# Optimization experiments

Measured on AMD Instinct MI355X. Metric: run time of the kernel, lower is better.

The kernel has to match this reference:

```python
import jax, jax.numpy as jnp
import numpy as np

HID = 64; N_LAYERS = 4; N_HEADS = 4; HEAD_DIM = 16; INTER = 32; MAXP = 1024; EPS = 1e-12


def setup_inputs() -> dict:
    key = jax.random.key(0)
    ks = iter(jax.random.split(key, 32))
    rn = lambda shape, s=0.02: jax.random.normal(next(ks), shape, jnp.float32) * s
    B, L = 32, 1024
    return {
        "features": jax.random.normal(next(ks), (B, L, HID), jnp.float32),
        "Wq": rn((N_LAYERS, HID, HID)), "bq": jnp.zeros((N_LAYERS, HID), jnp.float32),
        "Wk": rn((N_LAYERS, HID, HID)), "bk": jnp.zeros((N_LAYERS, HID), jnp.float32),
        "Wv": rn((N_LAYERS, HID, HID)), "bv": jnp.zeros((N_LAYERS, HID), jnp.float32),
        "Wo": rn((N_LAYERS, HID, HID)), "bo": jnp.zeros((N_LAYERS, HID), jnp.float32),
        "ln1_g": jnp.ones((N_LAYERS, HID), jnp.float32), "ln1_b": jnp.zeros((N_LAYERS, HID), jnp.float32),
        "Wi": rn((N_LAYERS, HID, INTER)), "bi": jnp.zeros((N_LAYERS, INTER), jnp.float32),
        "Wd": rn((N_LAYERS, INTER, HID)), "bd": jnp.zeros((N_LAYERS, HID), jnp.float32),
        "ln2_g": jnp.ones((N_LAYERS, HID), jnp.float32), "ln2_b": jnp.zeros((N_LAYERS, HID), jnp.float32),
        "rel_emb": rn((N_LAYERS, 2 * MAXP - 1, HEAD_DIM)),
        "fc_w": rn((HID, 6)), "fc_b": jnp.zeros((6,), jnp.float32),
    }


def _ln(x, g, b):
    m = jnp.mean(x, axis=-1, keepdims=True)
    v = jnp.mean((x - m) ** 2, axis=-1, keepdims=True)
    return (x - m) / jnp.sqrt(v + EPS) * g + b


def reference(features, Wq, bq, Wk, bk, Wv, bv, Wo, bo, ln1_g, ln1_b,
              Wi, bi, Wd, bd, ln2_g, ln2_b, rel_emb, fc_w, fc_b):
    B, L, _ = features.shape
    pos = jnp.arange(L)
    dist_idx = pos[:, None] - pos[None, :] + (MAXP - 1)  # [L, L] in [0, 2*MAXP-2]
    scale = np.float32(1.0 / np.sqrt(HEAD_DIM))

    def heads(t):  # [B,L,HID] -> [B,H,L,D]
        return t.reshape(B, L, N_HEADS, HEAD_DIM).transpose(0, 2, 1, 3)

    x = features
    for i in range(N_LAYERS):
        q = heads(x @ Wq[i] + bq[i])
        k = heads(x @ Wk[i] + bk[i])
        v = heads(x @ Wv[i] + bv[i])
        scores = jnp.einsum("bhld,bhrd->bhlr", q, k)
        pe = rel_emb[i][dist_idx]  # [L, L, D] relative_key positional embedding
        scores = scores + jnp.einsum("bhld,lrd->bhlr", q, pe)
        probs = jax.nn.softmax(scores * scale, axis=-1)
        ctx = jnp.einsum("bhlr,bhrd->bhld", probs, v).transpose(0, 2, 1, 3).reshape(B, L, HID)
        x = _ln(ctx @ Wo[i] + bo[i] + x, ln1_g[i], ln1_b[i])
        inter = jax.nn.gelu(x @ Wi[i] + bi[i], approximate=False)
        x = _ln(inter @ Wd[i] + bd[i] + x, ln2_g[i], ln2_b[i])
    return (x @ fc_w + fc_b)[:, 1:, :]
```

## Files before the change

kernel.cpp:

```cpp
#include <hip/hip_runtime.h>
#include <math.h>

static constexpr int Bc = 32;
static constexpr int Lc = 1024;

typedef _Float16 f16x4 __attribute__((ext_vector_type(4)));
typedef __fp16   h16x2 __attribute__((ext_vector_type(2)));
typedef float    f32x4 __attribute__((ext_vector_type(4)));

#define MFMA16(a, b, c) __builtin_amdgcn_mfma_f32_16x16x16f16((a), (b), (c), 0, 0, 0)

#if __has_builtin(__builtin_amdgcn_exp2f)
#define EXP2(x) __builtin_amdgcn_exp2f(x)
#else
#define EXP2(x) exp2f(x)
#endif

__global__ __launch_bounds__(256) void prep_kernel(
    const float* __restrict__ features, const float* __restrict__ rel,
    const float* __restrict__ Wq, const float* __restrict__ Wk,
    const float* __restrict__ Wv, const float* __restrict__ Wo,
    const float* __restrict__ Wi, const float* __restrict__ Wd,
    _Float16* __restrict__ xh, _Float16* __restrict__ relh,
    _Float16* __restrict__ wt)
{
    int i = blockIdx.x * 256 + threadIdx.x;
    {
        float4 v = ((const float4*)features)[i];
        h16x2 a = __builtin_amdgcn_cvt_pkrtz(v.x, v.y);
        h16x2 b = __builtin_amdgcn_cvt_pkrtz(v.z, v.w);
        f16x4 o; o[0] = a[0]; o[1] = a[1]; o[2] = b[0]; o[3] = b[1];
        ((f16x4*)xh)[i] = o;
    }
    if (i < 32752) {
        float4 v = ((const float4*)rel)[i];
        h16x2 a = __builtin_amdgcn_cvt_pkrtz(v.x, v.y);
        h16x2 b = __builtin_amdgcn_cvt_pkrtz(v.z, v.w);
        f16x4 o; o[0] = a[0]; o[1] = a[1]; o[2] = b[0]; o[3] = b[1];
        ((f16x4*)relh)[i] = o;
    }
    if (i < 65536) {
        int which = i >> 14, r = i & 16383;
        int m = r >> 12, k = (r >> 6) & 63, c = r & 63;
        const float* src = which == 0 ? Wq : which == 1 ? Wk : which == 2 ? Wv : Wo;
        wt[which * 16384 + m * 4096 + c * 64 + k] = (_Float16)src[r];
    } else if (i < 73728) {
        int r = i - 65536;
        int m = r >> 11, k = (r >> 5) & 63, c = r & 31;
        wt[65536 + m * 2048 + c * 64 + k] = (_Float16)Wi[r];
    } else if (i < 81920) {
        int r = i - 73728;
        int m = r >> 11, k = (r >> 6) & 31, c = r & 63;
        wt[73728 + m * 2048 + c * 32 + k] = (_Float16)Wd[r];
    }
}

__global__ __launch_bounds__(256) void qkv_kernel(
    const _Float16* __restrict__ xh,
    const _Float16* __restrict__ qT, const _Float16* __restrict__ kT,
    const _Float16* __restrict__ vT,
    const float* __restrict__ bq, const float* __restrict__ bk,
    const float* __restrict__ bv,
    _Float16* __restrict__ qo, _Float16* __restrict__ ko, _Float16* __restrict__ vt)
{
    const int t = threadIdx.x, wv = t >> 6, lane = t & 63, lo = lane & 15, hi = lane >> 4;
    const int row0 = blockIdx.x * 64 + wv * 16;
    const int b = row0 >> 10, l0 = row0 & 1023;

    f16x4 a[4];
    #pragma unroll
    for (int kk = 0; kk < 4; kk++)
        a[kk] = *(const f16x4*)(xh + (row0 + lo) * 64 + kk * 16 + 4 * hi);

    #pragma unroll
    for (int m = 0; m < 3; m++) {
        const _Float16* WT = m == 0 ? qT : m == 1 ? kT : vT;
        const float* bias  = m == 0 ? bq : m == 1 ? bk : bv;
        #pragma unroll
        for (int h = 0; h < 4; h++) {
            float bb = bias[h * 16 + lo];
            f32x4 acc = { bb, bb, bb, bb };
            #pragma unroll
            for (int kk = 0; kk < 4; kk++) {
                f16x4 bf = *(const f16x4*)(WT + (h * 16 + lo) * 64 + kk * 16 + 4 * hi);
                acc = MFMA16(a[kk], bf, acc);
            }
            int bh = b * 4 + h;
            if (m < 2) {
                _Float16* dst = (m == 0 ? qo : ko) + (bh * Lc + l0 + 4 * hi) * 16 + lo;
                dst[0]  = (_Float16)acc[0];
                dst[16] = (_Float16)acc[1];
                dst[32] = (_Float16)acc[2];
                dst[48] = (_Float16)acc[3];
            } else {
                h16x2 p0 = __builtin_amdgcn_cvt_pkrtz(acc[0], acc[1]);
                h16x2 p1 = __builtin_amdgcn_cvt_pkrtz(acc[2], acc[3]);
                f16x4 o; o[0] = p0[0]; o[1] = p0[1]; o[2] = p1[0]; o[3] = p1[1];
                *(f16x4*)(vt + (bh * 16 + lo) * Lc + l0 + 4 * hi) = o;
            }
        }
    }
}

__global__ __launch_bounds__(64) void attn_kernel(
    const _Float16* __restrict__ qg, const _Float16* __restrict__ kg,
    const _Float16* __restrict__ vtg, const _Float16* __restrict__ relh,
    _Float16* __restrict__ ctxh)
{
    __shared__ float Tl[4][16 * 52];
    const int lane = threadIdx.x & 63;
    const int bh = blockIdx.x & 127;
    const int l0 = (blockIdx.x >> 7) * 64;
    const int lo = lane & 15, hi = lane >> 4;

    const _Float16 qscale = (_Float16)0.36067376022224085f;
    f16x4 qf[4];
    #pragma unroll
    for (int i = 0; i < 4; i++) {
        qf[i] = *(const f16x4*)(qg + (bh * Lc + l0 + 16 * i + lo) * 16 + 4 * hi);
        #pragma unroll
        for (int j = 0; j < 4; j++) qf[i][j] *= qscale;
    }

    const int o = 12 + lo - 4 * hi;

    float* wrE[4]; float* wrO[4]; const float* rdE[4]; const float* rdO[4];
    #pragma unroll
    for (int i = 0; i < 4; i++) {
        float* ring = Tl[i];
        const int phiE = 16 * (i & 1);
        const int phiO = 16 - phiE;
        wrE[i] = ring + lo * 52 + phiE + 4 * hi;
        wrO[i] = ring + lo * 52 + phiO + 4 * hi;
        rdE[i] = ring + lo * 52 + phiE + o;
        rdO[i] = ring + lo * 52 + phiO + o;
    }

    const _Float16* rbase = relh + 4 * hi;
    auto ldrel = [&](int row) {
        row = row > 2046 ? 2046 : row;
        return *(const f16x4*)(rbase + row * 16);
    };
    auto t_store = [&](f16x4 rf, f16x4 q, float* wr, bool mir) {
        f32x4 z = { 0.f, 0.f, 0.f, 0.f };
        f32x4 tt = MFMA16(rf, q, z);
        *(f32x4*)(wr) = tt;
        if (mir) *(f32x4*)(wr + 32) = tt;
    };

    f16x4 P[6];
    #pragma unroll
    for (int k = 0; k < 6; k++) P[k] = ldrel(l0 + 16 * k + lo);
    #pragma unroll
    for (int i = 0; i < 4; i++) {
        t_store(P[i],     qf[i], wrE[i], (i & 1) == 0);
        t_store(P[i + 1], qf[i], wrO[i], (i & 1) == 1);
    }
    f16x4 rc0 = P[2], rc1 = P[3], rc2 = P[4], rc3 = P[5];
    int rrow = l0 + 96 + lo;

    f32x4 si[4];
    #pragma unroll
    for (int i = 0; i < 4; i++) {
        const float* rd = rdE[i];
        si[i][0] = rd[3]; si[i][1] = rd[2]; si[i][2] = rd[1]; si[i][3] = rd[0];
    }

    const _Float16* kp = kg  + (bh * Lc + 1008 + lo) * 16 + 4 * hi;
    const _Float16* vp = vtg + (bh * 16 + lo) * Lc + 1008 + 4 * hi;
    f16x4 kf0 = *(const f16x4*)kp;
    f16x4 vf0 = *(const f16x4*)vp;
    kp -= 256; vp -= 16;
    f16x4 kf1 = *(const f16x4*)kp;
    f16x4 vf1 = *(const f16x4*)vp;

    f32x4 ot[4], d[4];
    #pragma unroll
    for (int i = 0; i < 4; i++) {
        ot[i] = f32x4{ 0.f, 0.f, 0.f, 0.f };
        d[i]  = f32x4{ 0.f, 0.f, 0.f, 0.f };
    }

    #pragma unroll 2
    for (int t = 0; t < 64; ++t) {
        kp -= 256; vp -= 16;
        f16x4 kf2 = *(const f16x4*)kp;
        f16x4 vf2 = *(const f16x4*)vp;
        f16x4 r4 = ldrel(rrow); rrow += 16;

        f32x4 s[4];
        #pragma unroll
        for (int i = 0; i < 4; i++)
            s[i] = MFMA16(kf0, qf[i], si[i]);

        float e[4][4];
        #pragma unroll
        for (int i = 0; i < 4; i++)
            #pragma unroll
            for (int j = 0; j < 4; j++) {
                e[i][j] = EXP2(s[i][j]);
                d[i][j] += e[i][j];
            }

        t_store(rc0, qf[0], (t & 1) ? wrO[0] : wrE[0], (t & 1) == 0);
        t_store(rc1, qf[1], (t & 1) ? wrO[1] : wrE[1], (t & 1) == 1);
        t_store(rc2, qf[2], (t & 1) ? wrO[2] : wrE[2], (t & 1) == 0);
        t_store(rc3, qf[3], (t & 1) ? wrO[3] : wrE[3], (t & 1) == 1);

        #pragma unroll
        for (int i = 0; i < 4; i++) {
            const float* rd = (t & 1) ? rdE[i] : rdO[i];
            si[i][0] = rd[3]; si[i][1] = rd[2]; si[i][2] = rd[1]; si[i][3] = rd[0];
        }

        #pragma unroll
        for (int i = 0; i < 4; i++) {
            h16x2 pa = __builtin_amdgcn_cvt_pkrtz(e[i][0], e[i][1]);
            h16x2 pb = __builtin_amdgcn_cvt_pkrtz(e[i][2], e[i][3]);
            f16x4 pf; pf[0] = pa[0]; pf[1] = pa[1]; pf[2] = pb[0]; pf[3] = pb[1];
            ot[i] = MFMA16(vf0, pf, ot[i]);
        }

        kf0 = kf1; kf1 = kf2;
        vf0 = vf1; vf1 = vf2;
        rc0 = rc1; rc1 = rc2; rc2 = rc3; rc3 = r4;
    }

    const int b = bh >> 2, h = bh & 3;
    #pragma unroll
    for (int i = 0; i < 4; i++) {
        float den = (d[i][0] + d[i][1]) + (d[i][2] + d[i][3]);
        den += __shfl_xor(den, 16);
        den += __shfl_xor(den, 32);
        const float inv = 1.f / den;
        h16x2 o0 = __builtin_amdgcn_cvt_pkrtz(ot[i][0] * inv, ot[i][1] * inv);
        h16x2 o1 = __builtin_amdgcn_cvt_pkrtz(ot[i][2] * inv, ot[i][3] * inv);
        f16x4 o4; o4[0] = o0[0]; o4[1] = o0[1]; o4[2] = o1[0]; o4[3] = o1[1];
        *(f16x4*)(ctxh + (b * Lc + l0 + 16 * i + lo) * 64 + h * 16 + 4 * hi) = o4;
    }
}

__global__ __launch_bounds__(256) void tail_kernel(
    const _Float16* __restrict__ ctxh, const float* __restrict__ resid,
    const _Float16* __restrict__ woT, const float* __restrict__ bo,
    const float* __restrict__ g1, const float* __restrict__ b1,
    const _Float16* __restrict__ wiT, const float* __restrict__ bi,
    const _Float16* __restrict__ wdT, const float* __restrict__ bd,
    const float* __restrict__ g2, const float* __restrict__ b2,
    float* __restrict__ xout,
    int doq,
    const _Float16* __restrict__ qT, const _Float16* __restrict__ kT,
    const _Float16* __restrict__ vT,
    const float* __restrict__ bq, const float* __restrict__ bk,
    const float* __restrict__ bv,
    _Float16* __restrict__ qo, _Float16* __restrict__ ko, _Float16* __restrict__ vt)
{
    __shared__ _Float16 x1s[4][16 * 68];
    __shared__ _Float16 ins[4][16 * 36];
    const int t = threadIdx.x, wv = t >> 6, lane = t & 63, lo = lane & 15, hi = lane >> 4;
    const int row0 = blockIdx.x * 64 + wv * 16;

    f16x4 a[4];
    #pragma unroll
    for (int kk = 0; kk < 4; kk++)
        a[kk] = *(const f16x4*)(ctxh + (row0 + lo) * 64 + kk * 16 + 4 * hi);

    float c1[4][4];
    #pragma unroll
    for (int w = 0; w < 4; w++) {
        float bb = bo[w * 16 + lo];
        f32x4 acc;
        #pragma unroll
        for (int j = 0; j < 4; j++)
            acc[j] = bb + resid[(row0 + 4 * hi + j) * 64 + w * 16 + lo];
        #pragma unroll
        for (int kk = 0; kk < 4; kk++) {
            f16x4 bf = *(const f16x4*)(woT + (w * 16 + lo) * 64 + kk * 16 + 4 * hi);
            acc = MFMA16(a[kk], bf, acc);
        }
        #pragma unroll
        for (int j = 0; j < 4; j++) c1[w][j] = acc[j];
    }

    float x1[4][4];
    {
        float gg[4], bb2[4];
        #pragma unroll
        for (int w = 0; w < 4; w++) { gg[w] = g1[w * 16 + lo]; bb2[w] = b1[w * 16 + lo]; }
        #pragma unroll
        for (int j = 0; j < 4; j++) {
            float s = c1[0][j] + c1[1][j] + c1[2][j] + c1[3][j];
            float q = c1[0][j]*c1[0][j] + c1[1][j]*c1[1][j] + c1[2][j]*c1[2][j] + c1[3][j]*c1[3][j];
            #pragma unroll
            for (int off = 1; off < 16; off <<= 1) { s += __shfl_xor(s, off); q += __shfl_xor(q, off); }
            float m  = s * (1.f / 64.f);
            float vr = q * (1.f / 64.f) - m * m;
            float rs = rsqrtf(vr + 1e-12f);
            #pragma unroll
            for (int w = 0; w < 4; w++) x1[w][j] = (c1[w][j] - m) * rs * gg[w] + bb2[w];
        }
    }

    _Float16* xsp = x1s[wv];
    #pragma unroll
    for (int w = 0; w < 4; w++)
        #pragma unroll
        for (int j = 0; j < 4; j++)
            xsp[(4 * hi + j) * 68 + w * 16 + lo] = (_Float16)x1[w][j];
    f16x4 a2[4];
    #pragma unroll
    for (int kk = 0; kk < 4; kk++)
        a2[kk] = *(const f16x4*)(xsp + lo * 68 + kk * 16 + 4 * hi);

    float it[2][4];
    #pragma unroll
    for (int w = 0; w < 2; w++) {
        float bb = bi[w * 16 + lo];
        f32x4 acc = { bb, bb, bb, bb };
        #pragma unroll
        for (int kk = 0; kk < 4; kk++) {
            f16x4 bf = *(const f16x4*)(wiT + (w * 16 + lo) * 64 + kk * 16 + 4 * hi);
            acc = MFMA16(a2[kk], bf, acc);
        }
        #pragma unroll
        for (int j = 0; j < 4; j++) {
            float v = acc[j];
            it[w][j] = 0.5f * v * (1.f + erff(v * 0.70710678118654752f));
        }
    }

    _Float16* isp = ins[wv];
    #pragma unroll
    for (int w = 0; w < 2; w++)
        #pragma unroll
        for (int j = 0; j < 4; j++)
            isp[(4 * hi + j) * 36 + w * 16 + lo] = (_Float16)it[w][j];
    f16x4 a3[2];
    #pragma unroll
    for (int kk = 0; kk < 2; kk++)
        a3[kk] = *(const f16x4*)(isp + lo * 36 + kk * 16 + 4 * hi);

    float c2[4][4];
    #pragma unroll
    for (int w = 0; w < 4; w++) {
        float bb = bd[w * 16 + lo];
        f32x4 acc;
        #pragma unroll
        for (int j = 0; j < 4; j++) acc[j] = bb + x1[w][j];
        #pragma unroll
        for (int kk = 0; kk < 2; kk++) {
            f16x4 bf = *(const f16x4*)(wdT + (w * 16 + lo) * 32 + kk * 16 + 4 * hi);
            acc = MFMA16(a3[kk], bf, acc);
        }
        #pragma unroll
        for (int j = 0; j < 4; j++) c2[w][j] = acc[j];
    }

    float x2[4][4];
    {
        float gg[4], bb2[4];
        #pragma unroll
        for (int w = 0; w < 4; w++) { gg[w] = g2[w * 16 + lo]; bb2[w] = b2[w * 16 + lo]; }
        #pragma unroll
        for (int j = 0; j < 4; j++) {
            float s = c2[0][j] + c2[1][j] + c2[2][j] + c2[3][j];
            float q = c2[0][j]*c2[0][j] + c2[1][j]*c2[1][j] + c2[2][j]*c2[2][j] + c2[3][j]*c2[3][j];
            #pragma unroll
            for (int off = 1; off < 16; off <<= 1) { s += __shfl_xor(s, off); q += __shfl_xor(q, off); }
            float m  = s * (1.f / 64.f);
            float vr = q * (1.f / 64.f) - m * m;
            float rs = rsqrtf(vr + 1e-12f);
            #pragma unroll
            for (int w = 0; w < 4; w++) {
                float xv = (c2[w][j] - m) * rs * gg[w] + bb2[w];
                x2[w][j] = xv;
                xout[(row0 + 4 * hi + j) * 64 + w * 16 + lo] = xv;
            }
        }
    }

    if (!doq) return;

    #pragma unroll
    for (int w = 0; w < 4; w++)
        #pragma unroll
        for (int j = 0; j < 4; j++)
            xsp[(4 * hi + j) * 68 + w * 16 + lo] = (_Float16)x2[w][j];
    f16x4 aq[4];
    #pragma unroll
    for (int kk = 0; kk < 4; kk++)
        aq[kk] = *(const f16x4*)(xsp + lo * 68 + kk * 16 + 4 * hi);

    const int b = row0 >> 10, l0q = row0 & 1023;
    #pragma unroll
    for (int m = 0; m < 3; m++) {
        const _Float16* WT = m == 0 ? qT : m == 1 ? kT : vT;
        const float* bias  = m == 0 ? bq : m == 1 ? bk : bv;
        #pragma unroll
        for (int h = 0; h < 4; h++) {
            float bb = bias[h * 16 + lo];
            f32x4 acc = { bb, bb, bb, bb };
            #pragma unroll
            for (int kk = 0; kk < 4; kk++) {
                f16x4 bf = *(const f16x4*)(WT + (h * 16 + lo) * 64 + kk * 16 + 4 * hi);
                acc = MFMA16(aq[kk], bf, acc);
            }
            int bh = b * 4 + h;
            if (m < 2) {
                _Float16* dst = (m == 0 ? qo : ko) + (bh * Lc + l0q + 4 * hi) * 16 + lo;
                dst[0]  = (_Float16)acc[0];
                dst[16] = (_Float16)acc[1];
                dst[32] = (_Float16)acc[2];
                dst[48] = (_Float16)acc[3];
            } else {
                h16x2 p0 = __builtin_amdgcn_cvt_pkrtz(acc[0], acc[1]);
                h16x2 p1 = __builtin_amdgcn_cvt_pkrtz(acc[2], acc[3]);
                f16x4 o; o[0] = p0[0]; o[1] = p0[1]; o[2] = p1[0]; o[3] = p1[1];
                *(f16x4*)(vt + (bh * 16 + lo) * Lc + l0q + 4 * hi) = o;
            }
        }
    }
}

__global__ __launch_bounds__(256) void final_kernel(
    const float* __restrict__ x, const float* __restrict__ fcw,
    const float* __restrict__ fcb, float* __restrict__ out)
{
    int idx = blockIdx.x * 256 + threadIdx.x;
    if (idx >= Bc * 1023 * 6) return;
    int j = idx % 6;
    int rest = idx / 6;
    int l = rest % 1023 + 1;
    int b = rest / 1023;
    const float* xr = x + (b * Lc + l) * 64;
    float acc = fcb[j];
    for (int k = 0; k < 64; ++k) acc += xr[k] * fcw[k * 6 + j];
    out[idx] = acc;
}

extern "C" void kernel_launch(void* const* d_in, const int* in_sizes, int n_in,
                              void* d_out, int out_size, void* d_ws, size_t ws_size,
                              hipStream_t stream)
{
    (void)in_sizes; (void)n_in; (void)out_size; (void)ws_size;
    const float* features = (const float*)d_in[0];
    const float* Wq  = (const float*)d_in[1];
    const float* bq  = (const float*)d_in[2];
    const float* Wk  = (const float*)d_in[3];
    const float* bk  = (const float*)d_in[4];
    const float* Wv  = (const float*)d_in[5];
    const float* bv  = (const float*)d_in[6];
    const float* Wo  = (const float*)d_in[7];
    const float* bo  = (const float*)d_in[8];
    const float* g1  = (const float*)d_in[9];
    const float* b1  = (const float*)d_in[10];
    const float* Wi  = (const float*)d_in[11];
    const float* bi  = (const float*)d_in[12];
    const float* Wd  = (const float*)d_in[13];
    const float* bd  = (const float*)d_in[14];
    const float* g2  = (const float*)d_in[15];
    const float* b2  = (const float*)d_in[16];
    const float* rel = (const float*)d_in[17];
    const float* fcw = (const float*)d_in[18];
    const float* fcb = (const float*)d_in[19];
    float* out = (float*)d_out;

    char* ws = (char*)d_ws;
    float*    xbuf = (float*)(ws);
    _Float16* xh   = (_Float16*)(ws + ( 8u << 20));
    _Float16* ctxh = (_Float16*)(ws + (12u << 20));
    _Float16* qh   = (_Float16*)(ws + (16u << 20));
    _Float16* kh   = (_Float16*)(ws + (20u << 20));
    _Float16* vt   = (_Float16*)(ws + (24u << 20));
    _Float16* relh = (_Float16*)(ws + (28u << 20));
    _Float16* wt   = (_Float16*)(ws + (28u << 20) + (512u << 10));

    prep_kernel<<<2048, 256, 0, stream>>>(features, rel, Wq, Wk, Wv, Wo, Wi, Wd,
                                          xh, relh, wt);
    qkv_kernel<<<512, 256, 0, stream>>>(xh,
        wt, wt + 16384, wt + 32768, bq, bk, bv, qh, kh, vt);

    for (int i = 0; i < 4; ++i) {
        const float* resid = (i == 0) ? features : xbuf;
        int ni = i + 1;
        attn_kernel<<<2048, 64, 0, stream>>>(qh, kh, vt,
            relh + i * 2047 * 16, ctxh);
        tail_kernel<<<512, 256, 0, stream>>>(ctxh, resid,
            wt + 49152 + i * 4096, bo + i * 64, g1 + i * 64, b1 + i * 64,
            wt + 65536 + i * 2048, bi + i * 32,
            wt + 73728 + i * 2048, bd + i * 64, g2 + i * 64, b2 + i * 64,
            xbuf,
            (i < 3) ? 1 : 0,
            wt + ni * 4096, wt + 16384 + ni * 4096, wt + 32768 + ni * 4096,
            bq + ni * 64, bk + ni * 64, bv + ni * 64,
            qh, kh, vt);
    }
    final_kernel<<<768, 256, 0, stream>>>(xbuf, fcw, fcb, out);
}
```

Measured before the change: 299.3 us.

## Fuse attention and layer tail into one kernel with ping-pong QKV buffers

Merges the per-head attention kernel and the output/FFN/LayerNorm/next-QKV tail kernel into a single 256-thread layer kernel. Each of the four waves computes one head for the same 64-row tile and writes its context into shared memory, which the tail then reads, so the global ctx round trip and one launch per layer go away. Because blocks now write the next layer's Q/K/V while other blocks still read the current ones, the Q/K/V buffers are double-buffered. The cost is a larger shared-memory footprint per block and only 512 blocks of 256 threads, against 2048 single-wave attention blocks before, which may reduce occupancy and latency hiding in the attention loop.

```diff
diff --git a/kernel.cpp b/kernel.cpp
--- a/kernel.cpp
+++ b/kernel.cpp
@@ -102,146 +102,10 @@
     }
 }
 
-__global__ __launch_bounds__(64) void attn_kernel(
+__global__ __launch_bounds__(256) void layer_kernel(
     const _Float16* __restrict__ qg, const _Float16* __restrict__ kg,
     const _Float16* __restrict__ vtg, const _Float16* __restrict__ relh,
-    _Float16* __restrict__ ctxh)
-{
-    __shared__ float Tl[4][16 * 52];
-    const int lane = threadIdx.x & 63;
-    const int bh = blockIdx.x & 127;
-    const int l0 = (blockIdx.x >> 7) * 64;
-    const int lo = lane & 15, hi = lane >> 4;
-
-    const _Float16 qscale = (_Float16)0.36067376022224085f;
-    f16x4 qf[4];
-    #pragma unroll
-    for (int i = 0; i < 4; i++) {
-        qf[i] = *(const f16x4*)(qg + (bh * Lc + l0 + 16 * i + lo) * 16 + 4 * hi);
-        #pragma unroll
-        for (int j = 0; j < 4; j++) qf[i][j] *= qscale;
-    }
-
-    const int o = 12 + lo - 4 * hi;
-
-    float* wrE[4]; float* wrO[4]; const float* rdE[4]; const float* rdO[4];
-    #pragma unroll
-    for (int i = 0; i < 4; i++) {
-        float* ring = Tl[i];
-        const int phiE = 16 * (i & 1);
-        const int phiO = 16 - phiE;
-        wrE[i] = ring + lo * 52 + phiE + 4 * hi;
-        wrO[i] = ring + lo * 52 + phiO + 4 * hi;
-        rdE[i] = ring + lo * 52 + phiE + o;
-        rdO[i] = ring + lo * 52 + phiO + o;
-    }
-
-    const _Float16* rbase = relh + 4 * hi;
-    auto ldrel = [&](int row) {
-        row = row > 2046 ? 2046 : row;
-        return *(const f16x4*)(rbase + row * 16);
-    };
-    auto t_store = [&](f16x4 rf, f16x4 q, float* wr, bool mir) {
-        f32x4 z = { 0.f, 0.f, 0.f, 0.f };
-        f32x4 tt = MFMA16(rf, q, z);
-        *(f32x4*)(wr) = tt;
-        if (mir) *(f32x4*)(wr + 32) = tt;
-    };
-
-    f16x4 P[6];
-    #pragma unroll
-    for (int k = 0; k < 6; k++) P[k] = ldrel(l0 + 16 * k + lo);
-    #pragma unroll
-    for (int i = 0; i < 4; i++) {
-        t_store(P[i],     qf[i], wrE[i], (i & 1) == 0);
-        t_store(P[i + 1], qf[i], wrO[i], (i & 1) == 1);
-    }
-    f16x4 rc0 = P[2], rc1 = P[3], rc2 = P[4], rc3 = P[5];
-    int rrow = l0 + 96 + lo;
-
-    f32x4 si[4];
-    #pragma unroll
-    for (int i = 0; i < 4; i++) {
-        const float* rd = rdE[i];
-        si[i][0] = rd[3]; si[i][1] = rd[2]; si[i][2] = rd[1]; si[i][3] = rd[0];
-    }
-
-    const _Float16* kp = kg  + (bh * Lc + 1008 + lo) * 16 + 4 * hi;
-    const _Float16* vp = vtg + (bh * 16 + lo) * Lc + 1008 + 4 * hi;
-    f16x4 kf0 = *(const f16x4*)kp;
-    f16x4 vf0 = *(const f16x4*)vp;
-    kp -= 256; vp -= 16;
-    f16x4 kf1 = *(const f16x4*)kp;
-    f16x4 vf1 = *(const f16x4*)vp;
-
-    f32x4 ot[4], d[4];
-    #pragma unroll
-    for (int i = 0; i < 4; i++) {
-        ot[i] = f32x4{ 0.f, 0.f, 0.f, 0.f };
-        d[i]  = f32x4{ 0.f, 0.f, 0.f, 0.f };
-    }
-
-    #pragma unroll 2
-    for (int t = 0; t < 64; ++t) {
-        kp -= 256; vp -= 16;
-        f16x4 kf2 = *(const f16x4*)kp;
-        f16x4 vf2 = *(const f16x4*)vp;
-        f16x4 r4 = ldrel(rrow); rrow += 16;
-
-        f32x4 s[4];
-        #pragma unroll
-        for (int i = 0; i < 4; i++)
-            s[i] = MFMA16(kf0, qf[i], si[i]);
-
-        float e[4][4];
-        #pragma unroll
-        for (int i = 0; i < 4; i++)
-            #pragma unroll
-            for (int j = 0; j < 4; j++) {
-                e[i][j] = EXP2(s[i][j]);
-                d[i][j] += e[i][j];
-            }
-
-        t_store(rc0, qf[0], (t & 1) ? wrO[0] : wrE[0], (t & 1) == 0);
-        t_store(rc1, qf[1], (t & 1) ? wrO[1] : wrE[1], (t & 1) == 1);
-        t_store(rc2, qf[2], (t & 1) ? wrO[2] : wrE[2], (t & 1) == 0);
-        t_store(rc3, qf[3], (t & 1) ? wrO[3] : wrE[3], (t & 1) == 1);
-
-        #pragma unroll
-        for (int i = 0; i < 4; i++) {
-            const float* rd = (t & 1) ? rdE[i] : rdO[i];
-            si[i][0] = rd[3]; si[i][1] = rd[2]; si[i][2] = rd[1]; si[i][3] = rd[0];
-        }
-
-        #pragma unroll
-        for (int i = 0; i < 4; i++) {
-            h16x2 pa = __builtin_amdgcn_cvt_pkrtz(e[i][0], e[i][1]);
-            h16x2 pb = __builtin_amdgcn_cvt_pkrtz(e[i][2], e[i][3]);
-            f16x4 pf; pf[0] = pa[0]; pf[1] = pa[1]; pf[2] = pb[0]; pf[3] = pb[1];
-            ot[i] = MFMA16(vf0, pf, ot[i]);
-        }
-
-        kf0 = kf1; kf1 = kf2;
-        vf0 = vf1; vf1 = vf2;
-        rc0 = rc1; rc1 = rc2; rc2 = rc3; rc3 = r4;
-    }
-
-    const int b = bh >> 2, h = bh & 3;
-    #pragma unroll
-    for (int i = 0; i < 4; i++) {
-        float den = (d[i][0] + d[i][1]) + (d[i][2] + d[i][3]);
-        den += __shfl_xor(den, 16);
-        den += __shfl_xor(den, 32);
-        const float inv = 1.f / den;
-        h16x2 o0 = __builtin_amdgcn_cvt_pkrtz(ot[i][0] * inv, ot[i][1] * inv);
-        h16x2 o1 = __builtin_amdgcn_cvt_pkrtz(ot[i][2] * inv, ot[i][3] * inv);
-        f16x4 o4; o4[0] = o0[0]; o4[1] = o0[1]; o4[2] = o1[0]; o4[3] = o1[1];
-        *(f16x4*)(ctxh + (b * Lc + l0 + 16 * i + lo) * 64 + h * 16 + 4 * hi) = o4;
-    }
-}
-
-__global__ __launch_bounds__(256) void tail_kernel(
-    const _Float16* __restrict__ ctxh, const float* __restrict__ resid,
+    const float* __restrict__ resid,
     const _Float16* __restrict__ woT, const float* __restrict__ bo,
     const float* __restrict__ g1, const float* __restrict__ b1,
     const _Float16* __restrict__ wiT, const float* __restrict__ bi,
@@ -253,17 +117,153 @@
     const _Float16* __restrict__ vT,
     const float* __restrict__ bq, const float* __restrict__ bk,
     const float* __restrict__ bv,
-    _Float16* __restrict__ qo, _Float16* __restrict__ ko, _Float16* __restrict__ vt)
+    _Float16* __restrict__ qo, _Float16* __restrict__ ko, _Float16* __restrict__ vo)
 {
-    __shared__ _Float16 x1s[4][16 * 68];
-    __shared__ _Float16 ins[4][16 * 36];
-    const int t = threadIdx.x, wv = t >> 6, lane = t & 63, lo = lane & 15, hi = lane >> 4;
-    const int row0 = blockIdx.x * 64 + wv * 16;
+    __shared__ float Tmem[4 * 3328];
+    const int tid = threadIdx.x;
+    const int wv = tid >> 6, lane = tid & 63;
+    const int b  = blockIdx.x & 31;
+    const int l0 = (blockIdx.x >> 5) * 64;
+    const int bh = b * 4 + wv;
+    const int lo = lane & 15, hi = lane >> 4;
+    float* wbase = Tmem + wv * 3328;
+
+    {
+        const _Float16 qscale = (_Float16)0.36067376022224085f;
+        f16x4 qf[4];
+        #pragma unroll
+        for (int i = 0; i < 4; i++) {
+            qf[i] = *(const f16x4*)(qg + (bh * Lc + l0 + 16 * i + lo) * 16 + 4 * hi);
+            #pragma unroll
+            for (int j = 0; j < 4; j++) qf[i][j] *= qscale;
+        }
+
+        const int o = 12 + lo - 4 * hi;
+
+        float* wrE[4]; float* wrO[4]; const float* rdE[4]; const float* rdO[4];
+        #pragma unroll
+        for (int i = 0; i < 4; i++) {
+            float* ring = wbase + i * 832;
+            const int phiE = 16 * (i & 1);
+            const int phiO = 16 - phiE;
+            wrE[i] = ring + lo * 52 + phiE + 4 * hi;
+            wrO[i] = ring + lo * 52 + phiO + 4 * hi;
+            rdE[i] = ring + lo * 52 + phiE + o;
+            rdO[i] = ring + lo * 52 + phiO + o;
+        }
+
+        const _Float16* rbase = relh + 4 * hi;
+        auto ldrel = [&](int row) {
+            row = row > 2046 ? 2046 : row;
+            return *(const f16x4*)(rbase + row * 16);
+        };
+        auto t_store = [&](f16x4 rf, f16x4 q, float* wr, bool mir) {
+            f32x4 z = { 0.f, 0.f, 0.f, 0.f };
+            f32x4 tt = MFMA16(rf, q, z);
+            *(f32x4*)(wr) = tt;
+            if (mir) *(f32x4*)(wr + 32) = tt;
+        };
+
+        f16x4 P[6];
+        #pragma unroll
+        for (int k = 0; k < 6; k++) P[k] = ldrel(l0 + 16 * k + lo);
+        #pragma unroll
+        for (int i = 0; i < 4; i++) {
+            t_store(P[i],     qf[i], wrE[i], (i & 1) == 0);
+            t_store(P[i + 1], qf[i], wrO[i], (i & 1) == 1);
+        }
+        f16x4 rc0 = P[2], rc1 = P[3], rc2 = P[4], rc3 = P[5];
+        int rrow = l0 + 96 + lo;
+
+        f32x4 si[4];
+        #pragma unroll
+        for (int i = 0; i < 4; i++) {
+            const float* rd = rdE[i];
+            si[i][0] = rd[3]; si[i][1] = rd[2]; si[i][2] = rd[1]; si[i][3] = rd[0];
+        }
+
+        const _Float16* kp = kg  + (bh * Lc + 1008 + lo) * 16 + 4 * hi;
+        const _Float16* vp = vtg + (bh * 16 + lo) * Lc + 1008 + 4 * hi;
+        f16x4 kf0 = *(const f16x4*)kp;
+        f16x4 vf0 = *(const f16x4*)vp;
+        kp -= 256; vp -= 16;
+        f16x4 kf1 = *(const f16x4*)kp;
+        f16x4 vf1 = *(const f16x4*)vp;
+
+        f32x4 ot[4], d[4];
+        #pragma unroll
+        for (int i = 0; i < 4; i++) {
+            ot[i] = f32x4{ 0.f, 0.f, 0.f, 0.f };
+            d[i]  = f32x4{ 0.f, 0.f, 0.f, 0.f };
+        }
+
+        #pragma unroll 2
+        for (int t = 0; t < 64; ++t) {
+            kp -= 256; vp -= 16;
+            f16x4 kf2 = *(const f16x4*)kp;
+            f16x4 vf2 = *(const f16x4*)vp;
+            f16x4 r4 = ldrel(rrow); rrow += 16;
+
+            f32x4 s[4];
+            #pragma unroll
+            for (int i = 0; i < 4; i++)
+                s[i] = MFMA16(kf0, qf[i], si[i]);
+
+            float e[4][4];
+            #pragma unroll
+            for (int i = 0; i < 4; i++)
+                #pragma unroll
+                for (int j = 0; j < 4; j++) {
+                    e[i][j] = EXP2(s[i][j]);
+                    d[i][j] += e[i][j];
+                }
+
+            t_store(rc0, qf[0], (t & 1) ? wrO[0] : wrE[0], (t & 1) == 0);
+            t_store(rc1, qf[1], (t & 1) ? wrO[1] : wrE[1], (t & 1) == 1);
+            t_store(rc2, qf[2], (t & 1) ? wrO[2] : wrE[2], (t & 1) == 0);
+            t_store(rc3, qf[3], (t & 1) ? wrO[3] : wrE[3], (t & 1) == 1);
+
+            #pragma unroll
+            for (int i = 0; i < 4; i++) {
+                const float* rd = (t & 1) ? rdE[i] : rdO[i];
+                si[i][0] = rd[3]; si[i][1] = rd[2]; si[i][2] = rd[1]; si[i][3] = rd[0];
+            }
+
+            #pragma unroll
+            for (int i = 0; i < 4; i++) {
+                h16x2 pa = __builtin_amdgcn_cvt_pkrtz(e[i][0], e[i][1]);
+                h16x2 pb = __builtin_amdgcn_cvt_pkrtz(e[i][2], e[i][3]);
+                f16x4 pf; pf[0] = pa[0]; pf[1] = pa[1]; pf[2] = pb[0]; pf[3] = pb[1];
+                ot[i] = MFMA16(vf0, pf, ot[i]);
+            }
+
+            kf0 = kf1; kf1 = kf2;
+            vf0 = vf1; vf1 = vf2;
+            rc0 = rc1; rc1 = rc2; rc2 = rc3; rc3 = r4;
+        }
+
+        _Float16* ctxw = (_Float16*)wbase;
+        #pragma unroll
+        for (int i = 0; i < 4; i++) {
+            float den = (d[i][0] + d[i][1]) + (d[i][2] + d[i][3]);
+            den += __shfl_xor(den, 16);
+            den += __shfl_xor(den, 32);
+            const float inv = 1.f / den;
+            h16x2 o0 = __builtin_amdgcn_cvt_pkrtz(ot[i][0] * inv, ot[i][1] * inv);
+            h16x2 o1 = __builtin_amdgcn_cvt_pkrtz(ot[i][2] * inv, ot[i][3] * inv);
+            f16x4 o4; o4[0] = o0[0]; o4[1] = o0[1]; o4[2] = o1[0]; o4[3] = o1[1];
+            *(f16x4*)(ctxw + (16 * i + lo) * 16 + 4 * hi) = o4;
+        }
+    }
+    __syncthreads();
+
+    const _Float16* ctxs = (const _Float16*)Tmem;
+    const int row0g = b * Lc + l0 + wv * 16;
 
     f16x4 a[4];
     #pragma unroll
     for (int kk = 0; kk < 4; kk++)
-        a[kk] = *(const f16x4*)(ctxh + (row0 + lo) * 64 + kk * 16 + 4 * hi);
+        a[kk] = *(const f16x4*)(ctxs + kk * 6656 + (wv * 16 + lo) * 16 + 4 * hi);
 
     float c1[4][4];
     #pragma unroll
@@ -272,7 +272,7 @@
         f32x4 acc;
         #pragma unroll
         for (int j = 0; j < 4; j++)
-            acc[j] = bb + resid[(row0 + 4 * hi + j) * 64 + w * 16 + lo];
+            acc[j] = bb + resid[(row0g + 4 * hi + j) * 64 + w * 16 + lo];
         #pragma unroll
         for (int kk = 0; kk < 4; kk++) {
             f16x4 bf = *(const f16x4*)(woT + (w * 16 + lo) * 64 + kk * 16 + 4 * hi);
@@ -301,7 +301,9 @@
         }
     }
 
-    _Float16* xsp = x1s[wv];
+    _Float16* xsp = (_Float16*)(wbase + 512);
+    _Float16* isp = (_Float16*)(wbase + 512 + 544);
+
     #pragma unroll
     for (int w = 0; w < 4; w++)
         #pragma unroll
@@ -329,7 +331,6 @@
         }
     }
 
-    _Float16* isp = ins[wv];
     #pragma unroll
     for (int w = 0; w < 2; w++)
         #pragma unroll
@@ -374,7 +375,7 @@
             for (int w = 0; w < 4; w++) {
                 float xv = (c2[w][j] - m) * rs * gg[w] + bb2[w];
                 x2[w][j] = xv;
-                xout[(row0 + 4 * hi + j) * 64 + w * 16 + lo] = xv;
+                xout[(row0g + 4 * hi + j) * 64 + w * 16 + lo] = xv;
             }
         }
     }
@@ -391,7 +392,7 @@
     for (int kk = 0; kk < 4; kk++)
         aq[kk] = *(const f16x4*)(xsp + lo * 68 + kk * 16 + 4 * hi);
 
-    const int b = row0 >> 10, l0q = row0 & 1023;
+    const int bb_ = row0g >> 10, l0q = row0g & 1023;
     #pragma unroll
     for (int m = 0; m < 3; m++) {
         const _Float16* WT = m == 0 ? qT : m == 1 ? kT : vT;
@@ -405,9 +406,9 @@
                 f16x4 bf = *(const f16x4*)(WT + (h * 16 + lo) * 64 + kk * 16 + 4 * hi);
                 acc = MFMA16(aq[kk], bf, acc);
             }
-            int bh = b * 4 + h;
+            int bhn = bb_ * 4 + h;
             if (m < 2) {
-                _Float16* dst = (m == 0 ? qo : ko) + (bh * Lc + l0q + 4 * hi) * 16 + lo;
+                _Float16* dst = (m == 0 ? qo : ko) + (bhn * Lc + l0q + 4 * hi) * 16 + lo;
                 dst[0]  = (_Float16)acc[0];
                 dst[16] = (_Float16)acc[1];
                 dst[32] = (_Float16)acc[2];
@@ -416,7 +417,7 @@
                 h16x2 p0 = __builtin_amdgcn_cvt_pkrtz(acc[0], acc[1]);
                 h16x2 p1 = __builtin_amdgcn_cvt_pkrtz(acc[2], acc[3]);
                 f16x4 o; o[0] = p0[0]; o[1] = p0[1]; o[2] = p1[0]; o[3] = p1[1];
-                *(f16x4*)(vt + (bh * 16 + lo) * Lc + l0q + 4 * hi) = o;
+                *(f16x4*)(vo + (bhn * 16 + lo) * Lc + l0q + 4 * hi) = o;
             }
         }
     }
@@ -467,25 +468,33 @@
 
     char* ws = (char*)d_ws;
     float*    xbuf = (float*)(ws);
-    _Float16* xh   = (_Float16*)(ws + ( 8u << 20));
-    _Float16* ctxh = (_Float16*)(ws + (12u << 20));
-    _Float16* qh   = (_Float16*)(ws + (16u << 20));
-    _Float16* kh   = (_Float16*)(ws + (20u << 20));
-    _Float16* vt   = (_Float16*)(ws + (24u << 20));
-    _Float16* relh = (_Float16*)(ws + (28u << 20));
-    _Float16* wt   = (_Float16*)(ws + (28u << 20) + (512u << 10));
+    _Float16* qh1  = (_Float16*)(ws + ( 8u << 20));
+    _Float16* xh   = qh1;
+    _Float16* kh1  = (_Float16*)(ws + (12u << 20));
+    _Float16* vt1  = (_Float16*)(ws + (16u << 20));
+    _Float16* qh0  = (_Float16*)(ws + (20u << 20));
+    _Float16* kh0  = (_Float16*)(ws + (24u << 20));
+    _Float16* vt0  = (_Float16*)(ws + (28u << 20));
+    _Float16* relh = (_Float16*)(ws + (32u << 20));
+    _Float16* wt   = (_Float16*)(ws + (32u << 20) + (512u << 10));
 
     prep_kernel<<<2048, 256, 0, stream>>>(features, rel, Wq, Wk, Wv, Wo, Wi, Wd,
                                           xh, relh, wt);
     qkv_kernel<<<512, 256, 0, stream>>>(xh,
-        wt, wt + 16384, wt + 32768, bq, bk, bv, qh, kh, vt);
+        wt, wt + 16384, wt + 32768, bq, bk, bv, qh0, kh0, vt0);
 
     for (int i = 0; i < 4; ++i) {
         const float* resid = (i == 0) ? features : xbuf;
-        int ni = i + 1;
-        attn_kernel<<<2048, 64, 0, stream>>>(qh, kh, vt,
-            relh + i * 2047 * 16, ctxh);
-        tail_kernel<<<512, 256, 0, stream>>>(ctxh, resid,
+        const int ni = (i < 3) ? (i + 1) : 3;
+        const _Float16* qin = (i & 1) ? qh1 : qh0;
+        const _Float16* kin = (i & 1) ? kh1 : kh0;
+        const _Float16* vin = (i & 1) ? vt1 : vt0;
+        _Float16* qout = (i & 1) ? qh0 : qh1;
+        _Float16* kout = (i & 1) ? kh0 : kh1;
+        _Float16* vout = (i & 1) ? vt0 : vt1;
+
+        layer_kernel<<<512, 256, 0, stream>>>(qin, kin, vin,
+            relh + i * 2047 * 16, resid,
             wt + 49152 + i * 4096, bo + i * 64, g1 + i * 64, b1 + i * 64,
             wt + 65536 + i * 2048, bi + i * 32,
             wt + 73728 + i * 2048, bd + i * 64, g2 + i * 64, b2 + i * 64,
@@ -493,7 +502,7 @@
             (i < 3) ? 1 : 0,
             wt + ni * 4096, wt + 16384 + ni * 4096, wt + 32768 + ni * 4096,
             bq + ni * 64, bk + ni * 64, bv + ni * 64,
-            qh, kh, vt);
+            qout, kout, vout);
     }
     final_kernel<<<768, 256, 0, stream>>>(xbuf, fcw, fcb, out);
 }
```

New measurement: 262.8 us, median of 2. 1.14x faster.
